# Performance work log

Hardware: AMD Instinct MI355X
Metric: run time of the kernel (lower is better)

The kernel has to match this reference:

```python
import jax, jax.numpy as jnp
import numpy as np

NEG_SLOPE = 0.2


def _gatv2_hop(x_l, x_r, src, dst, att_k, bias_k, num_nodes, add_self_loops):
    # x_l, x_r: [N, H, C]; src/dst: [E] int; att_k: [H, C]; bias_k: [C]
    if add_self_loops:
        loop = jnp.arange(num_nodes, dtype=src.dtype)
        src = jnp.concatenate([src, loop])
        dst = jnp.concatenate([dst, loop])
    g = jax.nn.leaky_relu(x_l[src] + x_r[dst], NEG_SLOPE)      # [E, H, C]
    logit = jnp.einsum('ehc,hc->eh', g, att_k)                 # [E, H]
    m = jax.ops.segment_max(logit, dst, num_segments=num_nodes)  # [N, H]
    a = jnp.exp(logit - m[dst])
    denom = jax.ops.segment_sum(a, dst, num_segments=num_nodes)  # [N, H]
    alpha = a / denom[dst]                                     # [E, H]
    out = jax.ops.segment_sum(alpha[:, :, None] * x_l[src], dst,
                              num_segments=num_nodes)          # [N, H, C]
    return out.mean(axis=1) + bias_k                           # concat=False -> head mean


def setup_inputs() -> dict:
    key = jax.random.key(0)
    N, E, IN, H, C, K = 50000, 800000, 128, 4, 32, 3
    ks = jax.random.split(key, 16)
    x = jax.random.normal(ks[0], (N, IN), dtype=jnp.float32)
    edges = {}
    for k in range(K):
        src = jax.random.randint(ks[1 + 2 * k], (E,), 0, N, dtype=jnp.int32)
        off = jax.random.randint(ks[2 + 2 * k], (E,), 1, N, dtype=jnp.int32)
        dst = (src + off) % N  # guarantees no self-loops in the data
        edges[f'edge_index{k}'] = jnp.stack([src, dst])
    s = 1.0 / np.sqrt(IN)
    w_l = jax.random.normal(ks[7], (IN, H * C), dtype=jnp.float32) * s
    b_l = jax.random.normal(ks[8], (H * C,), dtype=jnp.float32) * 0.02
    w_r = jax.random.normal(ks[9], (IN, H * C), dtype=jnp.float32) * s
    b_r = jax.random.normal(ks[10], (H * C,), dtype=jnp.float32) * 0.02
    att = jax.random.normal(ks[11], (K, H, C), dtype=jnp.float32) * (1.0 / np.sqrt(C))
    conv_bias = jax.random.normal(ks[12], (K, C), dtype=jnp.float32) * 0.02
    gate_w = jax.random.normal(ks[13], (IN, K), dtype=jnp.float32) * s
    gate_b = jax.random.normal(ks[14], (K,), dtype=jnp.float32) * 0.02
    return dict(x=x, **edges, w_l=w_l, b_l=b_l, w_r=w_r, b_r=b_r, att=att,
                conv_bias=conv_bias, gate_w=gate_w, gate_b=gate_b)


def reference(x, edge_index0, edge_index1, edge_index2,
              w_l, b_l, w_r, b_r, att, conv_bias, gate_w, gate_b):
    N = x.shape[0]
    H, C = att.shape[1], att.shape[2]
    x_l = (x @ w_l + b_l).reshape(N, H, C)  # shared lin_l across hops
    x_r = (x @ w_r + b_r).reshape(N, H, C)  # shared lin_r across hops
    edges = [edge_index0, edge_index1, edge_index2]
    msgs = [
        _gatv2_hop(x_l, x_r, ei[0], ei[1], att[k], conv_bias[k], N,
                   add_self_loops=(k == 0))
        for k, ei in enumerate(edges)
    ]
    messages = jnp.stack(msgs, axis=1)                 # [N, K, C]
    weights = jax.nn.softmax(x @ gate_w + gate_b, -1)  # [N, K]
    return jnp.einsum('nkc,nk->nc', messages, weights)
```

## Files before the change

kernel.cpp:

```cpp
#include <hip/hip_runtime.h>
#include <math.h>

typedef unsigned int uint32;
typedef unsigned short u16;

#if __has_builtin(__builtin_amdgcn_exp2f)
#define EXP2F(x) __builtin_amdgcn_exp2f(x)
#else
#define EXP2F(x) exp2f(x)
#endif

#define LROWS 64
#define CHUNK 8192
#define CHUNK_SHIFT 13
#define NBUCK_MAX 512
#define LPB 384

typedef __attribute__((ext_vector_type(8))) short bf16x8;
typedef __attribute__((ext_vector_type(4))) float f32x4;

__device__ __forceinline__ u16 f2bf(float f) {
    uint32 u = __float_as_uint(f);
    u += 0x7fffu + ((u >> 16) & 1u);
    return (u16)(u >> 16);
}
__device__ __forceinline__ float bflo(uint32 v) { return __uint_as_float(v << 16); }
__device__ __forceinline__ float bfhij(uint32 v) { return __uint_as_float(v); }

template<int PAT>
__device__ __forceinline__ float swz(float v) {
    return __int_as_float(__builtin_amdgcn_ds_swizzle(__float_as_int(v), PAT));
}
template<int CTRL>
__device__ __forceinline__ float dppadd(float v) {
    int r = __builtin_amdgcn_update_dpp(0, __float_as_int(v), CTRL, 0xF, 0xF, true);
    return v + __int_as_float(r);
}

__device__ __forceinline__ void edge_decode(
    int t, int E, const int* __restrict__ e0, const int* __restrict__ e1,
    const int* __restrict__ e2, int& hop, int& src, int& dst)
{
    if (t < E)          { hop = 0; src = e0[t];         dst = e0[E + t]; }
    else if (t < 2 * E) { hop = 1; src = e1[t - E];     dst = e1[t]; }
    else if (t < 3 * E) { hop = 2; src = e2[t - 2 * E]; dst = e2[t - E]; }
    else                { hop = 0; src = t - 3 * E;     dst = src; }
}

__global__ __launch_bounds__(256) void wprep(
    const float* __restrict__ wl, const float* __restrict__ wr, u16* __restrict__ wfrag)
{
    int ct = blockIdx.x;
    int ks = threadIdx.x >> 6;
    int lane = threadIdx.x & 63;
    int g = lane >> 4, rr = lane & 15;
    int c = ct * 16 + rr;
    const float* w = (c < 128) ? wl : wr;
    int cc = c & 127;
    u16* o = wfrag + (((size_t)ct * 4 + ks) * 64 + lane) * 8;
#pragma unroll
    for (int i = 0; i < 8; ++i) {
        int k = ks * 32 + g * 4 + (i & 3) + ((i >> 2) << 4);
        o[i] = f2bf(w[k * 128 + cc]);
    }
}

__global__ __launch_bounds__(256) void fused_pre(
    const float* __restrict__ x, const u16* __restrict__ wfrag,
    const float* __restrict__ bl, const float* __restrict__ br,
    const float* __restrict__ gw, const float* __restrict__ gb,
    u16* __restrict__ xl, u16* __restrict__ xr, float* __restrict__ gate4,
    const int* __restrict__ e0, const int* __restrict__ e1, const int* __restrict__ e2,
    int* __restrict__ hist,
    int N, int E, int T, int LB, int NBUCK)
{
    __shared__ float4 sx[LROWS][32];
    __shared__ float gbuf[LROWS][3];
    __shared__ int lhist[NBUCK_MAX];

    if ((int)blockIdx.x >= LB) {
        int blk = (int)blockIdx.x - LB;
        int t0 = blk << CHUNK_SHIFT;
        for (int j = threadIdx.x; j < NBUCK; j += 256) lhist[j] = 0;
        __syncthreads();
        for (int it = 0; it < CHUNK / 256; ++it) {
            int t = t0 + it * 256 + (int)threadIdx.x;
            if (t < T) {
                int dst;
                if (t < E)          dst = e0[E + t];
                else if (t < 2 * E) dst = e1[t];
                else if (t < 3 * E) dst = e2[t - E];
                else                dst = t - 3 * E;
                atomicAdd(&lhist[dst >> 7], 1);
            }
        }
        __syncthreads();
        for (int j = threadIdx.x; j < NBUCK; j += 256)
            hist[(size_t)blk * NBUCK + j] = lhist[j];
        return;
    }
    int t = threadIdx.x;
    int r0 = blockIdx.x * LROWS;
    int nr = min(LROWS, N - r0);
    {
        const float4* xi = (const float4*)(x + (size_t)r0 * 128);
        for (int i = t; i < nr * 32; i += 256) ((float4*)sx)[i] = xi[i];
    }
    __syncthreads();
    int wv = t >> 6, lane = t & 63;
    int g = lane >> 4, rr = lane & 15;
    bf16x8 afr[4];
    {
        const float4* xrow = sx[wv * 16 + rr];
#pragma unroll
        for (int ks = 0; ks < 4; ++ks) {
            float4 u = xrow[ks * 8 + g];
            float4 v = xrow[ks * 8 + 4 + g];
            union { u16 h[8]; bf16x8 v8; } pk;
            pk.h[0] = f2bf(u.x); pk.h[1] = f2bf(u.y);
            pk.h[2] = f2bf(u.z); pk.h[3] = f2bf(u.w);
            pk.h[4] = f2bf(v.x); pk.h[5] = f2bf(v.y);
            pk.h[6] = f2bf(v.z); pk.h[7] = f2bf(v.w);
            afr[ks] = pk.v8;
        }
    }
    const bf16x8* wfp = (const bf16x8*)wfrag;
    for (int ct = 0; ct < 16; ++ct) {
        f32x4 acc = {0.f, 0.f, 0.f, 0.f};
#pragma unroll
        for (int ks = 0; ks < 4; ++ks) {
            bf16x8 bf = wfp[((ct * 4 + ks) << 6) + lane];
            acc = __builtin_amdgcn_mfma_f32_16x16x32_bf16(afr[ks], bf, acc, 0, 0, 0);
        }
        int c = ct * 16 + rr;
        float bv = (ct < 8) ? bl[c] : br[c - 128];
        u16* ob = (ct < 8) ? xl : xr;
        int cc = c & 127;
#pragma unroll
        for (int i = 0; i < 4; ++i) {
            int row = wv * 16 + g * 4 + i;
            if (row < nr)
                ob[(size_t)(r0 + row) * 128 + cc] = f2bf(acc[i] + bv);
        }
    }
    if (t < nr * 3) {
        int r = t / 3, k = t - 3 * r;
        float s = 0.f;
        const float4* xrow = sx[r];
#pragma unroll 4
        for (int i = 0; i < 32; ++i) {
            float4 v = xrow[i];
            s += v.x * gw[(4 * i + 0) * 3 + k] + v.y * gw[(4 * i + 1) * 3 + k]
               + v.z * gw[(4 * i + 2) * 3 + k] + v.w * gw[(4 * i + 3) * 3 + k];
        }
        gbuf[r][k] = s + gb[k];
    }
    __syncthreads();
    if (t < nr) {
        float s0 = gbuf[t][0], s1 = gbuf[t][1], s2 = gbuf[t][2];
        float mx = fmaxf(s0, fmaxf(s1, s2));
        float e0v = __expf(s0 - mx), e1v = __expf(s1 - mx), e2v = __expf(s2 - mx);
        float inv = 1.f / (e0v + e1v + e2v);
        *(float4*)(gate4 + (size_t)(r0 + t) * 4) = make_float4(e0v * inv, e1v * inv, e2v * inv, 0.f);
    }
}

__global__ __launch_bounds__(1024) void scan1h(const int* __restrict__ hist, int MH,
                                               int NBLKA, int NBUCK,
                                               int* __restrict__ histS, int* __restrict__ partials) {
    __shared__ int s[1024];
    int t = threadIdx.x;
    int i = blockIdx.x * 1024 + t;
    int v = 0;
    if (i < MH) {
        int bin = (int)((uint32)i / (uint32)NBLKA);
        int blk = i - bin * NBLKA;
        v = hist[(size_t)blk * NBUCK + bin];
    }
    s[t] = v;
    __syncthreads();
    for (int o = 1; o < 1024; o <<= 1) {
        int u = (t >= o) ? s[t - o] : 0;
        __syncthreads();
        s[t] += u;
        __syncthreads();
    }
    if (i < MH) histS[i] = s[t] - v;
    if (t == 1023) partials[blockIdx.x] = s[1023];
}

__global__ __launch_bounds__(1024) void scan2(int* __restrict__ partials, int G) {
    __shared__ int s[1024];
    int t = threadIdx.x;
    int v = (t < G) ? partials[t] : 0;
    s[t] = v;
    __syncthreads();
    for (int o = 1; o < 1024; o <<= 1) {
        int u = (t >= o) ? s[t - o] : 0;
        __syncthreads();
        s[t] += u;
        __syncthreads();
    }
    if (t < G) partials[t] = s[t] - v;
}

__global__ __launch_bounds__(512) void passA2(
    const int* __restrict__ e0, const int* __restrict__ e1, const int* __restrict__ e2,
    int E, int T, int NBLKA, int NBUCK,
    const int* __restrict__ hist, const int* __restrict__ histS,
    const int* __restrict__ partials,
    uint32* __restrict__ pairs)
{
    __shared__ int lscan[512];
    __shared__ int gbase[512];
    __shared__ uint32 lp[CHUNK];
    __shared__ u16 lb[CHUNK];
    int blk = blockIdx.x, tid = threadIdx.x;
    int t0 = blk << CHUNK_SHIFT;
    int vc = min(CHUNK, T - t0);
    int c = (tid < NBUCK) ? hist[(size_t)blk * NBUCK + tid] : 0;
    lscan[tid] = c;
    __syncthreads();
    for (int o = 1; o < 512; o <<= 1) {
        int u = (tid >= o) ? lscan[tid - o] : 0;
        __syncthreads();
        lscan[tid] += u;
        __syncthreads();
    }
    int excl = lscan[tid] - c;
    lscan[tid] = excl;
    if (tid < NBUCK) {
        int k = tid * NBLKA + blk;
        gbase[tid] = histS[k] + partials[k >> 10] - excl;
    }
    __syncthreads();
    for (int it = 0; it < CHUNK / 512; ++it) {
        int t = t0 + it * 512 + tid;
        if (t < T) {
            int hop, src, dst;
            edge_decode(t, E, e0, e1, e2, hop, src, dst);
            int bin = dst >> 7;
            int j = atomicAdd(&lscan[bin], 1);
            lp[j] = (uint32)src | ((uint32)((dst & 127) * 3 + hop) << 16);
            lb[j] = (u16)bin;
        }
    }
    __syncthreads();
    for (int j = tid; j < vc; j += 512)
        pairs[gbase[lb[j]] + j] = lp[j];
}

__global__ __launch_bounds__(512) void passB(
    const uint32* __restrict__ pairs, const int* __restrict__ histS,
    const int* __restrict__ partials, u16* __restrict__ csr, int* __restrict__ offsets,
    int T, int M, int NBLKA, int NBUCK) {
    __shared__ int cnt[LPB];
    __shared__ int scn[512];
    int b = blockIdx.x;
    int tid = threadIdx.x;
    int k0 = b * NBLKA;
    int bbase = histS[k0] + partials[k0 >> 10];
    int bend;
    if (b == NBUCK - 1) bend = T;
    else { int k1 = k0 + NBLKA; bend = histS[k1] + partials[k1 >> 10]; }
    if (b == 0 && tid == 0) offsets[M] = T;

    if (tid < LPB) cnt[tid] = 0;
    __syncthreads();
    for (int p = bbase + tid; p < bend; p += 512)
        atomicAdd(&cnt[pairs[p] >> 16], 1);
    __syncthreads();
    int c = (tid < LPB) ? cnt[tid] : 0;
    scn[tid] = c;
    __syncthreads();
    for (int o = 1; o < 512; o <<= 1) {
        int u = (tid >= o) ? scn[tid - o] : 0;
        __syncthreads();
        scn[tid] += u;
        __syncthreads();
    }
    int excl = scn[tid] - c;
    int nlists = min(LPB, M - b * LPB);
    if (tid < nlists) offsets[b * LPB + tid] = bbase + excl;
    __syncthreads();
    if (tid < LPB) cnt[tid] = excl;
    __syncthreads();
    for (int p = bbase + tid; p < bend; p += 512) {
        uint32 pr = pairs[p];
        int pos = bbase + atomicAdd(&cnt[pr >> 16], 1);
        csr[pos] = (u16)pr;
    }
}

__global__ __launch_bounds__(192) void node_hop(
    const uint2* __restrict__ xlv,
    const uint2* __restrict__ xrv,
    const u16* __restrict__ csr,
    const int* __restrict__ offsets,
    const float* __restrict__ att,
    const float* __restrict__ bias,
    const float* __restrict__ gate4,
    float* __restrict__ out,
    int N, int M)
{
    const float L2E = 1.44269504088896f;
    __shared__ float4 smsg[3][8];
    int n = blockIdx.x;
    int h = threadIdx.x >> 6;
    int lane = threadIdx.x & 63;
    int i = 3 * n + h;
    int half = lane >> 5, l5 = lane & 31;

    uint2 rv = xrv[(size_t)n * 32 + l5];
    float4 r4;
    r4.x = bflo(rv.x); r4.y = bfhij(rv.x);
    r4.z = bflo(rv.y); r4.w = bfhij(rv.y);
    float4 a4 = ((const float4*)(att + h * 128))[l5];
    float a6x = 0.6f * L2E * a4.x, a6y = 0.6f * L2E * a4.y;
    float a6z = 0.6f * L2E * a4.z, a6w = 0.6f * L2E * a4.w;
    float a4x = 0.4f * L2E * a4.x, a4y = 0.4f * L2E * a4.y;
    float a4z = 0.4f * L2E * a4.z, a4w = 0.4f * L2E * a4.w;
    int beg = offsets[i];
    int end = offsets[i + 1];

    float d = 0.f, acc0 = 0.f, acc1 = 0.f, acc2 = 0.f, acc3 = 0.f;
    int e = beg;
    int sA = csr[beg + half];
    int sB = csr[beg + 2 + half];
    uint2 lvA = xlv[sA * 32 + l5];
    uint2 lvB = xlv[sB * 32 + l5];
    for (; e + 4 <= end; e += 4) {
        uint2 cvA = lvA, cvB = lvB;
        sA = csr[e + 4 + half];
        sB = csr[e + 6 + half];
        lvA = xlv[sA * 32 + l5];
        lvB = xlv[sB * 32 + l5];
        float lxA0 = bflo(cvA.x), lxA1 = bfhij(cvA.x);
        float lxA2 = bflo(cvA.y), lxA3 = bfhij(cvA.y);
        float lxB0 = bflo(cvB.x), lxB1 = bfhij(cvB.x);
        float lxB2 = bflo(cvB.y), lxB3 = bfhij(cvB.y);
        float gA0 = lxA0 + r4.x, gA1 = lxA1 + r4.y;
        float gA2 = lxA2 + r4.z, gA3 = lxA3 + r4.w;
        float gB0 = lxB0 + r4.x, gB1 = lxB1 + r4.y;
        float gB2 = lxB2 + r4.z, gB3 = lxB3 + r4.w;
        float pA = a6x * gA0;
        pA = fmaf(a4x, fabsf(gA0), pA);
        pA = fmaf(a6y, gA1, pA);
        pA = fmaf(a4y, fabsf(gA1), pA);
        pA = fmaf(a6z, gA2, pA);
        pA = fmaf(a4z, fabsf(gA2), pA);
        pA = fmaf(a6w, gA3, pA);
        pA = fmaf(a4w, fabsf(gA3), pA);
        float pB = a6x * gB0;
        pB = fmaf(a4x, fabsf(gB0), pB);
        pB = fmaf(a6y, gB1, pB);
        pB = fmaf(a4y, fabsf(gB1), pB);
        pB = fmaf(a6z, gB2, pB);
        pB = fmaf(a4z, fabsf(gB2), pB);
        pB = fmaf(a6w, gB3, pB);
        pB = fmaf(a4w, fabsf(gB3), pB);
        pA = dppadd<0xB1>(pA);
        pB = dppadd<0xB1>(pB);
        pA = dppadd<0x4E>(pA);
        pB = dppadd<0x4E>(pB);
        pA = dppadd<0x141>(pA);
        pB = dppadd<0x141>(pB);
        float wvA = EXP2F(pA);
        float wvB = EXP2F(pB);
        d += wvA + wvB;
        acc0 = fmaf(wvA, lxA0, acc0);
        acc1 = fmaf(wvA, lxA1, acc1);
        acc2 = fmaf(wvA, lxA2, acc2);
        acc3 = fmaf(wvA, lxA3, acc3);
        acc0 = fmaf(wvB, lxB0, acc0);
        acc1 = fmaf(wvB, lxB1, acc1);
        acc2 = fmaf(wvB, lxB2, acc2);
        acc3 = fmaf(wvB, lxB3, acc3);
    }
    int rem = end - e;
    if (rem > 0) {
        int e1i = end - 1;
        int s1 = csr[min(e + half, e1i)];
        int s2 = csr[min(e + 2 + half, e1i)];
        uint2 cvA = xlv[s1 * 32 + l5];
        uint2 cvB = xlv[s2 * 32 + l5];
        bool vA = (e + half) < end;
        bool vB = (e + 2 + half) < end;
        float lxA0 = bflo(cvA.x), lxA1 = bfhij(cvA.x);
        float lxA2 = bflo(cvA.y), lxA3 = bfhij(cvA.y);
        float lxB0 = bflo(cvB.x), lxB1 = bfhij(cvB.x);
        float lxB2 = bflo(cvB.y), lxB3 = bfhij(cvB.y);
        float gA0 = lxA0 + r4.x, gA1 = lxA1 + r4.y;
        float gA2 = lxA2 + r4.z, gA3 = lxA3 + r4.w;
        float gB0 = lxB0 + r4.x, gB1 = lxB1 + r4.y;
        float gB2 = lxB2 + r4.z, gB3 = lxB3 + r4.w;
        float pA = a6x * gA0;
        pA = fmaf(a4x, fabsf(gA0), pA);
        pA = fmaf(a6y, gA1, pA);
        pA = fmaf(a4y, fabsf(gA1), pA);
        pA = fmaf(a6z, gA2, pA);
        pA = fmaf(a4z, fabsf(gA2), pA);
        pA = fmaf(a6w, gA3, pA);
        pA = fmaf(a4w, fabsf(gA3), pA);
        float pB = a6x * gB0;
        pB = fmaf(a4x, fabsf(gB0), pB);
        pB = fmaf(a6y, gB1, pB);
        pB = fmaf(a4y, fabsf(gB1), pB);
        pB = fmaf(a6z, gB2, pB);
        pB = fmaf(a4z, fabsf(gB2), pB);
        pB = fmaf(a6w, gB3, pB);
        pB = fmaf(a4w, fabsf(gB3), pB);
        pA = dppadd<0xB1>(pA);
        pB = dppadd<0xB1>(pB);
        pA = dppadd<0x4E>(pA);
        pB = dppadd<0x4E>(pB);
        pA = dppadd<0x141>(pA);
        pB = dppadd<0x141>(pB);
        float wvA = EXP2F(pA);
        float wvB = EXP2F(pB);
        wvA = vA ? wvA : 0.f;
        wvB = vB ? wvB : 0.f;
        d += wvA + wvB;
        acc0 = fmaf(wvA, lxA0, acc0);
        acc1 = fmaf(wvA, lxA1, acc1);
        acc2 = fmaf(wvA, lxA2, acc2);
        acc3 = fmaf(wvA, lxA3, acc3);
        acc0 = fmaf(wvB, lxB0, acc0);
        acc1 = fmaf(wvB, lxB1, acc1);
        acc2 = fmaf(wvB, lxB2, acc2);
        acc3 = fmaf(wvB, lxB3, acc3);
    }
    d += __shfl_xor(d, 32);
    acc0 += __shfl_xor(acc0, 32);
    acc1 += __shfl_xor(acc1, 32);
    acc2 += __shfl_xor(acc2, 32);
    acc3 += __shfl_xor(acc3, 32);
    float inv = (d > 0.f) ? (1.0f / d) : 0.f;
    float q0 = acc0 * inv, q1 = acc1 * inv, q2 = acc2 * inv, q3 = acc3 * inv;
    q0 += swz<0x201F>(q0);  q0 += swz<0x401F>(q0);
    q1 += swz<0x201F>(q1);  q1 += swz<0x401F>(q1);
    q2 += swz<0x201F>(q2);  q2 += swz<0x401F>(q2);
    q3 += swz<0x201F>(q3);  q3 += swz<0x401F>(q3);
    if (lane < 8) {
        float4 b4 = ((const float4*)(bias + h * 32))[lane];
        smsg[h][lane] = make_float4(fmaf(q0, 0.25f, b4.x), fmaf(q1, 0.25f, b4.y),
                                    fmaf(q2, 0.25f, b4.z), fmaf(q3, 0.25f, b4.w));
    }
    __syncthreads();
    if (threadIdx.x < 8) {
        int c = threadIdx.x;
        float4 g = ((const float4*)gate4)[n];
        float4 m0 = smsg[0][c], m1 = smsg[1][c], m2 = smsg[2][c];
        float4 o;
        o.x = g.x * m0.x + g.y * m1.x + g.z * m2.x;
        o.y = g.x * m0.y + g.y * m1.y + g.z * m2.y;
        o.z = g.x * m0.z + g.y * m1.z + g.z * m2.z;
        o.w = g.x * m0.w + g.y * m1.w + g.z * m2.w;
        ((float4*)(out + (size_t)n * 32))[c] = o;
    }
}

extern "C" void kernel_launch(void* const* d_in, const int* in_sizes, int n_in,
                              void* d_out, int out_size, void* d_ws, size_t ws_size,
                              hipStream_t stream) {
    const float* x  = (const float*)d_in[0];
    const int* e0 = (const int*)d_in[1];
    const int* e1 = (const int*)d_in[2];
    const int* e2 = (const int*)d_in[3];
    const float* wl = (const float*)d_in[4];
    const float* bl = (const float*)d_in[5];
    const float* wr = (const float*)d_in[6];
    const float* br = (const float*)d_in[7];
    const float* att = (const float*)d_in[8];
    const float* cb  = (const float*)d_in[9];
    const float* gw  = (const float*)d_in[10];
    const float* gb  = (const float*)d_in[11];

    int N = in_sizes[0] / 128;
    int E = in_sizes[1] / 2;
    float* out = (float*)d_out;

    int M = 3 * N;
    int T = 3 * E + N;
    int NBUCK = (N + 127) >> 7;
    int NBLKA = (T + CHUNK - 1) / CHUNK;
    int MH = NBUCK * NBLKA;

    char* ws = (char*)d_ws;
    u16* xl      = (u16*)ws;   ws += (size_t)N * 128 * 2;
    u16* xr      = (u16*)ws;   ws += (size_t)N * 128 * 2;
    float* gate4 = (float*)ws; ws += (size_t)N * 4 * 4;
    int* offsets  = (int*)ws; ws += (size_t)(M + 1) * 4;
    int* hist     = (int*)ws; ws += (size_t)MH * 4;
    int* histS    = (int*)ws; ws += (size_t)MH * 4;
    int* partials = (int*)ws; ws += 4096;
    u16* csr_src  = (u16*)ws; ws += (size_t)(T + 8) * 2;
    u16* wfrag    = (u16*)ws; ws += (size_t)16 * 4 * 64 * 8 * 2;
    uint32* pairs = (uint32*)(((uintptr_t)ws + 63) & ~(uintptr_t)63);

    int LB = (N + LROWS - 1) / LROWS;
    wprep<<<16, 256, 0, stream>>>(wl, wr, wfrag);
    fused_pre<<<LB + NBLKA, 256, 0, stream>>>(x, wfrag, bl, br, gw, gb, xl, xr, gate4,
                                              e0, e1, e2, hist, N, E, T, LB, NBUCK);
    int GH = (MH + 1023) / 1024;
    scan1h<<<GH, 1024, 0, stream>>>(hist, MH, NBLKA, NBUCK, histS, partials);
    scan2<<<1, 1024, 0, stream>>>(partials, GH);
    passA2<<<NBLKA, 512, 0, stream>>>(e0, e1, e2, E, T, NBLKA, NBUCK,
                                      hist, histS, partials, pairs);
    passB<<<NBUCK, 512, 0, stream>>>(pairs, histS, partials, csr_src, offsets,
                                     T, M, NBLKA, NBUCK);
    node_hop<<<N, 192, 0, stream>>>(
        (const uint2*)xl, (const uint2*)xr, csr_src, offsets, att, cb, gate4, out, N, M);
}
```

Baseline: 190.7 us.

## Use 16-byte loads with 16 lanes per edge and four edges in flight

The node_hop kernel now reads each source row with 16 lanes doing 16-byte loads instead of 32 lanes doing 8-byte loads, so a wavefront covers four edges per load instead of two. The main loop is unrolled to 16 edges per iteration with four prefetched rows, which raises memory-level parallelism. Per-lane work doubles to 8 channels, and the final reductions are reworked to match. This costs more registers per thread, adds a wider tail loop, and means up to 16 entries of the CSR index array can be read ahead, so its padding grows.

New measurement: 179.6 us. -5.8%, faster.

```diff
diff --git a/kernel.cpp b/kernel.cpp
--- a/kernel.cpp
+++ b/kernel.cpp
@@ -292,9 +292,38 @@
     }
 }
 
+#define NH_CHAIN(cv, wv_)                                              \
+    {                                                                  \
+        float lx[8] = {bflo(cv.x), bfhij(cv.x), bflo(cv.y), bfhij(cv.y), \
+                       bflo(cv.z), bfhij(cv.z), bflo(cv.w), bfhij(cv.w)}; \
+        float p = 0.f;                                                 \
+        _Pragma("unroll")                                              \
+        for (int j = 0; j < 8; ++j) {                                  \
+            float g_ = lx[j] + rr[j];                                  \
+            p = fmaf(a6[j], g_, p);                                    \
+            p = fmaf(a4[j], fabsf(g_), p);                             \
+        }                                                              \
+        p = dppadd<0xB1>(p);                                           \
+        p = dppadd<0x4E>(p);                                           \
+        wv_ = EXP2F(p);                                                \
+        lx0_ = lx[0]; lx1_ = lx[1]; lx2_ = lx[2]; lx3_ = lx[3];        \
+        lx4_ = lx[4]; lx5_ = lx[5]; lx6_ = lx[6]; lx7_ = lx[7];        \
+    }
+#define NH_ACCUM(wv_)                                                  \
+    {                                                                  \
+        d += wv_;                                                      \
+        acc[0] = fmaf(wv_, lx0_, acc[0]);                              \
+        acc[1] = fmaf(wv_, lx1_, acc[1]);                              \
+        acc[2] = fmaf(wv_, lx2_, acc[2]);                              \
+        acc[3] = fmaf(wv_, lx3_, acc[3]);                              \
+        acc[4] = fmaf(wv_, lx4_, acc[4]);                              \
+        acc[5] = fmaf(wv_, lx5_, acc[5]);                              \
+        acc[6] = fmaf(wv_, lx6_, acc[6]);                              \
+        acc[7] = fmaf(wv_, lx7_, acc[7]);                              \
+    }
 __global__ __launch_bounds__(192) void node_hop(
-    const uint2* __restrict__ xlv,
-    const uint2* __restrict__ xrv,
+    const uint4* __restrict__ xlv,
+    const uint4* __restrict__ xrv,
     const u16* __restrict__ csr,
     const int* __restrict__ offsets,
     const float* __restrict__ att,
@@ -309,142 +338,94 @@
     int h = threadIdx.x >> 6;
     int lane = threadIdx.x & 63;
     int i = 3 * n + h;
-    int half = lane >> 5, l5 = lane & 31;
-
-    uint2 rv = xrv[(size_t)n * 32 + l5];
-    float4 r4;
-    r4.x = bflo(rv.x); r4.y = bfhij(rv.x);
-    r4.z = bflo(rv.y); r4.w = bfhij(rv.y);
-    float4 a4 = ((const float4*)(att + h * 128))[l5];
-    float a6x = 0.6f * L2E * a4.x, a6y = 0.6f * L2E * a4.y;
-    float a6z = 0.6f * L2E * a4.z, a6w = 0.6f * L2E * a4.w;
-    float a4x = 0.4f * L2E * a4.x, a4y = 0.4f * L2E * a4.y;
-    float a4z = 0.4f * L2E * a4.z, a4w = 0.4f * L2E * a4.w;
+    int q = lane >> 4, m = lane & 15;
+
+    uint4 rv = xrv[(size_t)n * 16 + m];
+    float rr[8] = {bflo(rv.x), bfhij(rv.x), bflo(rv.y), bfhij(rv.y),
+                   bflo(rv.z), bfhij(rv.z), bflo(rv.w), bfhij(rv.w)};
+    float4 aA = ((const float4*)(att + h * 128))[2 * m];
+    float4 aB = ((const float4*)(att + h * 128))[2 * m + 1];
+    float av[8] = {aA.x, aA.y, aA.z, aA.w, aB.x, aB.y, aB.z, aB.w};
+    float a6[8], a4[8];
+#pragma unroll
+    for (int j = 0; j < 8; ++j) {
+        a6[j] = 0.6f * L2E * av[j];
+        a4[j] = 0.4f * L2E * av[j];
+    }
     int beg = offsets[i];
     int end = offsets[i + 1];
 
-    float d = 0.f, acc0 = 0.f, acc1 = 0.f, acc2 = 0.f, acc3 = 0.f;
+    float d = 0.f;
+    float acc[8];
+#pragma unroll
+    for (int j = 0; j < 8; ++j) acc[j] = 0.f;
+    float lx0_, lx1_, lx2_, lx3_, lx4_, lx5_, lx6_, lx7_;
     int e = beg;
-    int sA = csr[beg + half];
-    int sB = csr[beg + 2 + half];
-    uint2 lvA = xlv[sA * 32 + l5];
-    uint2 lvB = xlv[sB * 32 + l5];
-    for (; e + 4 <= end; e += 4) {
-        uint2 cvA = lvA, cvB = lvB;
-        sA = csr[e + 4 + half];
-        sB = csr[e + 6 + half];
-        lvA = xlv[sA * 32 + l5];
-        lvB = xlv[sB * 32 + l5];
-        float lxA0 = bflo(cvA.x), lxA1 = bfhij(cvA.x);
-        float lxA2 = bflo(cvA.y), lxA3 = bfhij(cvA.y);
-        float lxB0 = bflo(cvB.x), lxB1 = bfhij(cvB.x);
-        float lxB2 = bflo(cvB.y), lxB3 = bfhij(cvB.y);
-        float gA0 = lxA0 + r4.x, gA1 = lxA1 + r4.y;
-        float gA2 = lxA2 + r4.z, gA3 = lxA3 + r4.w;
-        float gB0 = lxB0 + r4.x, gB1 = lxB1 + r4.y;
-        float gB2 = lxB2 + r4.z, gB3 = lxB3 + r4.w;
-        float pA = a6x * gA0;
-        pA = fmaf(a4x, fabsf(gA0), pA);
-        pA = fmaf(a6y, gA1, pA);
-        pA = fmaf(a4y, fabsf(gA1), pA);
-        pA = fmaf(a6z, gA2, pA);
-        pA = fmaf(a4z, fabsf(gA2), pA);
-        pA = fmaf(a6w, gA3, pA);
-        pA = fmaf(a4w, fabsf(gA3), pA);
-        float pB = a6x * gB0;
-        pB = fmaf(a4x, fabsf(gB0), pB);
-        pB = fmaf(a6y, gB1, pB);
-        pB = fmaf(a4y, fabsf(gB1), pB);
-        pB = fmaf(a6z, gB2, pB);
-        pB = fmaf(a4z, fabsf(gB2), pB);
-        pB = fmaf(a6w, gB3, pB);
-        pB = fmaf(a4w, fabsf(gB3), pB);
-        pA = dppadd<0xB1>(pA);
-        pB = dppadd<0xB1>(pB);
-        pA = dppadd<0x4E>(pA);
-        pB = dppadd<0x4E>(pB);
-        pA = dppadd<0x141>(pA);
-        pB = dppadd<0x141>(pB);
-        float wvA = EXP2F(pA);
-        float wvB = EXP2F(pB);
-        d += wvA + wvB;
-        acc0 = fmaf(wvA, lxA0, acc0);
-        acc1 = fmaf(wvA, lxA1, acc1);
-        acc2 = fmaf(wvA, lxA2, acc2);
-        acc3 = fmaf(wvA, lxA3, acc3);
-        acc0 = fmaf(wvB, lxB0, acc0);
-        acc1 = fmaf(wvB, lxB1, acc1);
-        acc2 = fmaf(wvB, lxB2, acc2);
-        acc3 = fmaf(wvB, lxB3, acc3);
-    }
-    int rem = end - e;
-    if (rem > 0) {
+    if (e + 16 <= end) {
+        int sA = csr[e + q];
+        int sB = csr[e + 4 + q];
+        int sC = csr[e + 8 + q];
+        int sD = csr[e + 12 + q];
+        uint4 lvA = xlv[sA * 16 + m];
+        uint4 lvB = xlv[sB * 16 + m];
+        uint4 lvC = xlv[sC * 16 + m];
+        uint4 lvD = xlv[sD * 16 + m];
+        for (; e + 16 <= end; e += 16) {
+            uint4 cvA = lvA, cvB = lvB, cvC = lvC, cvD = lvD;
+            sA = csr[e + 16 + q];
+            sB = csr[e + 20 + q];
+            sC = csr[e + 24 + q];
+            sD = csr[e + 28 + q];
+            lvA = xlv[sA * 16 + m];
+            lvB = xlv[sB * 16 + m];
+            lvC = xlv[sC * 16 + m];
+            lvD = xlv[sD * 16 + m];
+            float wvv;
+            NH_CHAIN(cvA, wvv); NH_ACCUM(wvv);
+            NH_CHAIN(cvB, wvv); NH_ACCUM(wvv);
+            NH_CHAIN(cvC, wvv); NH_ACCUM(wvv);
+            NH_CHAIN(cvD, wvv); NH_ACCUM(wvv);
+        }
+    }
+    for (; e < end; e += 8) {
         int e1i = end - 1;
-        int s1 = csr[min(e + half, e1i)];
-        int s2 = csr[min(e + 2 + half, e1i)];
-        uint2 cvA = xlv[s1 * 32 + l5];
-        uint2 cvB = xlv[s2 * 32 + l5];
-        bool vA = (e + half) < end;
-        bool vB = (e + 2 + half) < end;
-        float lxA0 = bflo(cvA.x), lxA1 = bfhij(cvA.x);
-        float lxA2 = bflo(cvA.y), lxA3 = bfhij(cvA.y);
-        float lxB0 = bflo(cvB.x), lxB1 = bfhij(cvB.x);
-        float lxB2 = bflo(cvB.y), lxB3 = bfhij(cvB.y);
-        float gA0 = lxA0 + r4.x, gA1 = lxA1 + r4.y;
-        float gA2 = lxA2 + r4.z, gA3 = lxA3 + r4.w;
-        float gB0 = lxB0 + r4.x, gB1 = lxB1 + r4.y;
-        float gB2 = lxB2 + r4.z, gB3 = lxB3 + r4.w;
-        float pA = a6x * gA0;
-        pA = fmaf(a4x, fabsf(gA0), pA);
-        pA = fmaf(a6y, gA1, pA);
-        pA = fmaf(a4y, fabsf(gA1), pA);
-        pA = fmaf(a6z, gA2, pA);
-        pA = fmaf(a4z, fabsf(gA2), pA);
-        pA = fmaf(a6w, gA3, pA);
-        pA = fmaf(a4w, fabsf(gA3), pA);
-        float pB = a6x * gB0;
-        pB = fmaf(a4x, fabsf(gB0), pB);
-        pB = fmaf(a6y, gB1, pB);
-        pB = fmaf(a4y, fabsf(gB1), pB);
-        pB = fmaf(a6z, gB2, pB);
-        pB = fmaf(a4z, fabsf(gB2), pB);
-        pB = fmaf(a6w, gB3, pB);
-        pB = fmaf(a4w, fabsf(gB3), pB);
-        pA = dppadd<0xB1>(pA);
-        pB = dppadd<0xB1>(pB);
-        pA = dppadd<0x4E>(pA);
-        pB = dppadd<0x4E>(pB);
-        pA = dppadd<0x141>(pA);
-        pB = dppadd<0x141>(pB);
-        float wvA = EXP2F(pA);
-        float wvB = EXP2F(pB);
-        wvA = vA ? wvA : 0.f;
-        wvB = vB ? wvB : 0.f;
-        d += wvA + wvB;
-        acc0 = fmaf(wvA, lxA0, acc0);
-        acc1 = fmaf(wvA, lxA1, acc1);
-        acc2 = fmaf(wvA, lxA2, acc2);
-        acc3 = fmaf(wvA, lxA3, acc3);
-        acc0 = fmaf(wvB, lxB0, acc0);
-        acc1 = fmaf(wvB, lxB1, acc1);
-        acc2 = fmaf(wvB, lxB2, acc2);
-        acc3 = fmaf(wvB, lxB3, acc3);
-    }
-    d += __shfl_xor(d, 32);
-    acc0 += __shfl_xor(acc0, 32);
-    acc1 += __shfl_xor(acc1, 32);
-    acc2 += __shfl_xor(acc2, 32);
-    acc3 += __shfl_xor(acc3, 32);
+        int s1 = csr[min(e + q, e1i)];
+        int s2 = csr[min(e + 4 + q, e1i)];
+        uint4 cvA = xlv[s1 * 16 + m];
+        uint4 cvB = xlv[s2 * 16 + m];
+        bool vA = (e + q) < end;
+        bool vB = (e + 4 + q) < end;
+        float wvv;
+        NH_CHAIN(cvA, wvv);
+        wvv = vA ? wvv : 0.f;
+        NH_ACCUM(wvv);
+        NH_CHAIN(cvB, wvv);
+        wvv = vB ? wvv : 0.f;
+        NH_ACCUM(wvv);
+    }
+    d += swz<0x401F>(d);  d += __shfl_xor(d, 32);
+#pragma unroll
+    for (int j = 0; j < 8; ++j) {
+        acc[j] += swz<0x401F>(acc[j]);
+        acc[j] += __shfl_xor(acc[j], 32);
+    }
     float inv = (d > 0.f) ? (1.0f / d) : 0.f;
-    float q0 = acc0 * inv, q1 = acc1 * inv, q2 = acc2 * inv, q3 = acc3 * inv;
-    q0 += swz<0x201F>(q0);  q0 += swz<0x401F>(q0);
-    q1 += swz<0x201F>(q1);  q1 += swz<0x401F>(q1);
-    q2 += swz<0x201F>(q2);  q2 += swz<0x401F>(q2);
-    q3 += swz<0x201F>(q3);  q3 += swz<0x401F>(q3);
-    if (lane < 8) {
-        float4 b4 = ((const float4*)(bias + h * 32))[lane];
-        smsg[h][lane] = make_float4(fmaf(q0, 0.25f, b4.x), fmaf(q1, 0.25f, b4.y),
-                                    fmaf(q2, 0.25f, b4.z), fmaf(q3, 0.25f, b4.w));
+    float qv[8];
+#pragma unroll
+    for (int j = 0; j < 8; ++j) {
+        qv[j] = acc[j] * inv;
+        qv[j] += swz<0x101F>(qv[j]);
+        qv[j] += swz<0x201F>(qv[j]);
+    }
+    if (lane < 4) {
+        const float4* bp = (const float4*)(bias + h * 32);
+        float4 b1 = bp[2 * lane], b2 = bp[2 * lane + 1];
+        smsg[h][2 * lane] = make_float4(
+            fmaf(qv[0], 0.25f, b1.x), fmaf(qv[1], 0.25f, b1.y),
+            fmaf(qv[2], 0.25f, b1.z), fmaf(qv[3], 0.25f, b1.w));
+        smsg[h][2 * lane + 1] = make_float4(
+            fmaf(qv[4], 0.25f, b2.x), fmaf(qv[5], 0.25f, b2.y),
+            fmaf(qv[6], 0.25f, b2.z), fmaf(qv[7], 0.25f, b2.w));
     }
     __syncthreads();
     if (threadIdx.x < 8) {
@@ -494,7 +475,7 @@
     int* hist     = (int*)ws; ws += (size_t)MH * 4;
     int* histS    = (int*)ws; ws += (size_t)MH * 4;
     int* partials = (int*)ws; ws += 4096;
-    u16* csr_src  = (u16*)ws; ws += (size_t)(T + 8) * 2;
+    u16* csr_src  = (u16*)ws; ws += (size_t)(T + 16) * 2;
     u16* wfrag    = (u16*)ws; ws += (size_t)16 * 4 * 64 * 8 * 2;
     uint32* pairs = (uint32*)(((uintptr_t)ws + 63) & ~(uintptr_t)63);
 
@@ -510,5 +491,5 @@
     passB<<<NBUCK, 512, 0, stream>>>(pairs, histS, partials, csr_src, offsets,
                                      T, M, NBLKA, NBUCK);
     node_hop<<<N, 192, 0, stream>>>(
-        (const uint2*)xl, (const uint2*)xr, csr_src, offsets, att, cb, gate4, out, N, M);
-}
+        (const uint4*)xl, (const uint4*)xr, csr_src, offsets, att, cb, gate4, out, N, M);
+}
```
